# Kernel tuning notes

Measured on AMD Instinct MI355X. Metric: run time of the kernel, lower is better.

## Reference

```python
import jax, jax.numpy as jnp
import numpy as np

N_CELLS = 100000
IN_CH = 64
N_EDGES = 1280000


def setup_inputs() -> dict:
    key = jax.random.key(0)
    k1, k2, k3, k4, k5 = jax.random.split(key, 5)
    x_source = jax.random.normal(k1, (N_CELLS, IN_CH), dtype=jnp.float32)
    att_weight = jax.random.normal(k2, (2 * IN_CH,), dtype=jnp.float32)
    nbhd_values = jax.random.uniform(k3, (N_EDGES,), dtype=jnp.float32)
    target_index_i = jnp.sort(jax.random.randint(k4, (N_EDGES,), 0, N_CELLS))
    source_index_j = jax.random.randint(k5, (N_EDGES,), 0, N_CELLS)
    return {
        "x_source": x_source,
        "att_weight": att_weight,
        "nbhd_values": nbhd_values,
        "target_index_i": target_index_i,
        "source_index_j": source_index_j,
    }


def reference(x_source, att_weight, nbhd_values, target_index_i, source_index_j):
    # gather per-message endpoint features: [E, C] each
    x_src_msg = x_source[source_index_j]
    x_tgt_msg = x_source[target_index_i]  # x_target is None -> use x_source
    # attention: elu(cat([src, tgt]) @ w) -> [E]
    att = jax.nn.elu(
        jnp.concatenate([x_src_msg, x_tgt_msg], axis=1) @ att_weight
    )
    # modulate sparse neighborhood values by attention, scale messages
    vals = nbhd_values * att  # [E]
    x_message = vals[:, None] * x_src_msg  # [E, C]
    # scatter-sum into target cells: [N, C]
    return jax.ops.segment_sum(x_message, target_index_i, num_segments=N_CELLS)
```

## Files before the change

kernel.cpp:

```cpp
#include <hip/hip_runtime.h>

#define N_CELLS 100000
#define IN_CH 64
#define N_EDGES 1280000

__global__ void __launch_bounds__(256) score_kernel(
    const float* __restrict__ x, const float* __restrict__ w,
    float* __restrict__ s_src, float* __restrict__ s_tgt, int n_cells) {
    int gid  = blockIdx.x * blockDim.x + threadIdx.x;
    int wave = gid >> 6;
    int lane = threadIdx.x & 63;
    int grp  = lane >> 4;
    int sub  = lane & 15;
    int cell = wave * 4 + grp;

    float4 xv = make_float4(0.f, 0.f, 0.f, 0.f);
    if (cell < n_cells)
        xv = *(const float4*)&x[(((unsigned)cell << 6) | ((unsigned)sub << 2))];
    const float4* w4 = (const float4*)w;
    float4 wa = w4[sub];
    float4 wb = w4[16 + sub];
    float a = xv.x * wa.x + xv.y * wa.y + xv.z * wa.z + xv.w * wa.w;
    float b = xv.x * wb.x + xv.y * wb.y + xv.z * wb.z + xv.w * wb.w;
#pragma unroll
    for (int off = 8; off; off >>= 1) {
        a += __shfl_xor(a, off, 64);
        b += __shfl_xor(b, off, 64);
    }
    if (sub == 0 && cell < n_cells) {
        s_src[cell] = a;
        s_tgt[cell] = b;
    }
}

__global__ void __launch_bounds__(256) rowstart_kernel(
    const int* __restrict__ tgt, int* __restrict__ row_start,
    int n_edges, int n_cells) {
    int e = blockIdx.x * blockDim.x + threadIdx.x;
    if (e >= n_edges) return;
    int t = tgt[e];
    int prev = (e == 0) ? -1 : tgt[e - 1];
    for (int c = prev + 1; c <= t; ++c) row_start[c] = e;
    if (e == n_edges - 1) {
        for (int c = t + 1; c <= n_cells; ++c) row_start[c] = n_edges;
    }
}

__global__ void __launch_bounds__(256) agg_kernel(
    const float* __restrict__ x, const int* __restrict__ src,
    const float* __restrict__ nbhd,
    const float* __restrict__ s_src, const float* __restrict__ s_tgt,
    const int* __restrict__ row_start,
    float* __restrict__ out, int n_cells) {
    int gid  = blockIdx.x * blockDim.x + threadIdx.x;
    int cell = gid >> 6;
    int lane = threadIdx.x & 63;
    if (cell >= n_cells) return;
    int grp = lane >> 4;
    int sub = lane & 15;
    unsigned suboff = (unsigned)sub << 2;

    int lo = row_start[cell];
    int hi = row_start[cell + 1];
    float sti = s_tgt[cell];

    float4 acc = make_float4(0.f, 0.f, 0.f, 0.f);
    for (int base = lo; base < hi; base += 64) {
        int cnt = hi - base;
        if (cnt > 64) cnt = 64;
        int   j = 0;
        float v = 0.f;
        if (lane < cnt) {
            j = src[base + lane];
            float a = s_src[j] + sti;
            v = nbhd[base + lane] * (a > 0.f ? a : expm1f(a));
        }
        int t = 0;
        for (; t + 8 <= cnt; t += 8) {
            int   j0 = __shfl(j, t + grp, 64);
            float v0 = __shfl(v, t + grp, 64);
            int   j1 = __shfl(j, t + 4 + grp, 64);
            float v1 = __shfl(v, t + 4 + grp, 64);
            float4 x0 = *(const float4*)&x[(((unsigned)j0 << 6) | suboff)];
            float4 x1 = *(const float4*)&x[(((unsigned)j1 << 6) | suboff)];
            acc.x = fmaf(v0, x0.x, acc.x);
            acc.y = fmaf(v0, x0.y, acc.y);
            acc.z = fmaf(v0, x0.z, acc.z);
            acc.w = fmaf(v0, x0.w, acc.w);
            acc.x = fmaf(v1, x1.x, acc.x);
            acc.y = fmaf(v1, x1.y, acc.y);
            acc.z = fmaf(v1, x1.z, acc.z);
            acc.w = fmaf(v1, x1.w, acc.w);
        }
        for (; t < cnt; t += 4) {
            int   jt = __shfl(j, t + grp, 64);
            float vt = __shfl(v, t + grp, 64);
            float4 xt = *(const float4*)&x[(((unsigned)jt << 6) | suboff)];
            acc.x = fmaf(vt, xt.x, acc.x);
            acc.y = fmaf(vt, xt.y, acc.y);
            acc.z = fmaf(vt, xt.z, acc.z);
            acc.w = fmaf(vt, xt.w, acc.w);
        }
    }
#pragma unroll
    for (int off = 16; off <= 32; off <<= 1) {
        acc.x += __shfl_xor(acc.x, off, 64);
        acc.y += __shfl_xor(acc.y, off, 64);
        acc.z += __shfl_xor(acc.z, off, 64);
        acc.w += __shfl_xor(acc.w, off, 64);
    }
    if (grp == 0)
        *(float4*)&out[(((unsigned)cell << 6) | suboff)] = acc;
}

extern "C" void kernel_launch(void* const* d_in, const int* in_sizes, int n_in,
                              void* d_out, int out_size, void* d_ws, size_t ws_size,
                              hipStream_t stream) {
    const float* x    = (const float*)d_in[0];
    const float* w    = (const float*)d_in[1];
    const float* nbhd = (const float*)d_in[2];
    const int*   tgt  = (const int*)d_in[3];
    const int*   src  = (const int*)d_in[4];
    float*       out  = (float*)d_out;

    float* s_src     = (float*)d_ws;
    float* s_tgt     = s_src + N_CELLS;
    int*   row_start = (int*)(s_tgt + N_CELLS);

    {
        int threads = 256;
        int blocks  = (N_CELLS * 16 + threads - 1) / threads;
        score_kernel<<<blocks, threads, 0, stream>>>(x, w, s_src, s_tgt, N_CELLS);
    }
    {
        int threads = 256;
        int blocks  = (N_EDGES + threads - 1) / threads;
        rowstart_kernel<<<blocks, threads, 0, stream>>>(tgt, row_start, N_EDGES, N_CELLS);
    }
    {
        int threads = 256;
        int blocks  = (N_CELLS * 64 + threads - 1) / threads;
        agg_kernel<<<blocks, threads, 0, stream>>>(x, src, nbhd, s_src, s_tgt,
                                                   row_start, out, N_CELLS);
    }
}
```

Measured before the change: 65.40 us.

## Process four cells per wave with 16-lane groups in aggregation kernel

```diff
diff --git a/kernel.cpp b/kernel.cpp
--- a/kernel.cpp
+++ b/kernel.cpp
@@ -38,8 +38,10 @@
     int n_edges, int n_cells) {
     int e = blockIdx.x * blockDim.x + threadIdx.x;
     if (e >= n_edges) return;
+    int lane = threadIdx.x & 63;
     int t = tgt[e];
-    int prev = (e == 0) ? -1 : tgt[e - 1];
+    int prev = __shfl_up(t, 1, 64);
+    if (lane == 0) prev = (e == 0) ? -1 : tgt[e - 1];
     for (int c = prev + 1; c <= t; ++c) row_start[c] = e;
     if (e == n_edges - 1) {
         for (int c = t + 1; c <= n_cells; ++c) row_start[c] = n_edges;
@@ -53,63 +55,64 @@
     const int* __restrict__ row_start,
     float* __restrict__ out, int n_cells) {
     int gid  = blockIdx.x * blockDim.x + threadIdx.x;
-    int cell = gid >> 6;
     int lane = threadIdx.x & 63;
-    if (cell >= n_cells) return;
-    int grp = lane >> 4;
-    int sub = lane & 15;
+    int grp  = lane >> 4;
+    int sub  = lane & 15;
+    int cell = (gid >> 6) * 4 + grp;
     unsigned suboff = (unsigned)sub << 2;
+    int gbase = grp << 4;
 
-    int lo = row_start[cell];
-    int hi = row_start[cell + 1];
-    float sti = s_tgt[cell];
+    int lo = 0, hi = 0;
+    float sti = 0.f;
+    if (cell < n_cells) {
+        lo  = row_start[cell];
+        hi  = row_start[cell + 1];
+        sti = s_tgt[cell];
+    }
 
     float4 acc = make_float4(0.f, 0.f, 0.f, 0.f);
-    for (int base = lo; base < hi; base += 64) {
+    for (int base = lo; base < hi; base += 16) {
         int cnt = hi - base;
-        if (cnt > 64) cnt = 64;
+        if (cnt > 16) cnt = 16;
         int   j = 0;
         float v = 0.f;
-        if (lane < cnt) {
-            j = src[base + lane];
+        if (sub < cnt) {
+            j = src[base + sub];
             float a = s_src[j] + sti;
-            v = nbhd[base + lane] * (a > 0.f ? a : expm1f(a));
+            v = nbhd[base + sub] * (a > 0.f ? a : expm1f(a));
         }
         int t = 0;
-        for (; t + 8 <= cnt; t += 8) {
-            int   j0 = __shfl(j, t + grp, 64);
-            float v0 = __shfl(v, t + grp, 64);
-            int   j1 = __shfl(j, t + 4 + grp, 64);
-            float v1 = __shfl(v, t + 4 + grp, 64);
+        for (; t + 4 <= cnt; t += 4) {
+            int   j0 = __shfl(j, gbase + t,     64);
+            int   j1 = __shfl(j, gbase + t + 1, 64);
+            int   j2 = __shfl(j, gbase + t + 2, 64);
+            int   j3 = __shfl(j, gbase + t + 3, 64);
+            float v0 = __shfl(v, gbase + t,     64);
+            float v1 = __shfl(v, gbase + t + 1, 64);
+            float v2 = __shfl(v, gbase + t + 2, 64);
+            float v3 = __shfl(v, gbase + t + 3, 64);
             float4 x0 = *(const float4*)&x[(((unsigned)j0 << 6) | suboff)];
             float4 x1 = *(const float4*)&x[(((unsigned)j1 << 6) | suboff)];
-            acc.x = fmaf(v0, x0.x, acc.x);
-            acc.y = fmaf(v0, x0.y, acc.y);
-            acc.z = fmaf(v0, x0.z, acc.z);
-            acc.w = fmaf(v0, x0.w, acc.w);
-            acc.x = fmaf(v1, x1.x, acc.x);
-            acc.y = fmaf(v1, x1.y, acc.y);
-            acc.z = fmaf(v1, x1.z, acc.z);
-            acc.w = fmaf(v1, x1.w, acc.w);
+            float4 x2 = *(const float4*)&x[(((unsigned)j2 << 6) | suboff)];
+            float4 x3 = *(const float4*)&x[(((unsigned)j3 << 6) | suboff)];
+            acc.x = fmaf(v0, x0.x, acc.x); acc.y = fmaf(v0, x0.y, acc.y);
+            acc.z = fmaf(v0, x0.z, acc.z); acc.w = fmaf(v0, x0.w, acc.w);
+            acc.x = fmaf(v1, x1.x, acc.x); acc.y = fmaf(v1, x1.y, acc.y);
+            acc.z = fmaf(v1, x1.z, acc.z); acc.w = fmaf(v1, x1.w, acc.w);
+            acc.x = fmaf(v2, x2.x, acc.x); acc.y = fmaf(v2, x2.y, acc.y);
+            acc.z = fmaf(v2, x2.z, acc.z); acc.w = fmaf(v2, x2.w, acc.w);
+            acc.x = fmaf(v3, x3.x, acc.x); acc.y = fmaf(v3, x3.y, acc.y);
+            acc.z = fmaf(v3, x3.z, acc.z); acc.w = fmaf(v3, x3.w, acc.w);
         }
-        for (; t < cnt; t += 4) {
-            int   jt = __shfl(j, t + grp, 64);
-            float vt = __shfl(v, t + grp, 64);
+        for (; t < cnt; ++t) {
+            int   jt = __shfl(j, gbase + t, 64);
+            float vt = __shfl(v, gbase + t, 64);
             float4 xt = *(const float4*)&x[(((unsigned)jt << 6) | suboff)];
-            acc.x = fmaf(vt, xt.x, acc.x);
-            acc.y = fmaf(vt, xt.y, acc.y);
-            acc.z = fmaf(vt, xt.z, acc.z);
-            acc.w = fmaf(vt, xt.w, acc.w);
+            acc.x = fmaf(vt, xt.x, acc.x); acc.y = fmaf(vt, xt.y, acc.y);
+            acc.z = fmaf(vt, xt.z, acc.z); acc.w = fmaf(vt, xt.w, acc.w);
         }
     }
-#pragma unroll
-    for (int off = 16; off <= 32; off <<= 1) {
-        acc.x += __shfl_xor(acc.x, off, 64);
-        acc.y += __shfl_xor(acc.y, off, 64);
-        acc.z += __shfl_xor(acc.z, off, 64);
-        acc.w += __shfl_xor(acc.w, off, 64);
-    }
-    if (grp == 0)
+    if (cell < n_cells)
         *(float4*)&out[(((unsigned)cell << 6) | suboff)] = acc;
 }
 
@@ -139,7 +142,7 @@
     }
     {
         int threads = 256;
-        int blocks  = (N_CELLS * 64 + threads - 1) / threads;
+        int blocks  = (N_CELLS * 16 + threads - 1) / threads;
         agg_kernel<<<blocks, threads, 0, stream>>>(x, src, nbhd, s_src, s_tgt,
                                                    row_start, out, N_CELLS);
     }
```

Result: no change. 64.45 us (-1.5%).
